# Performance work log

Measured on AMD Instinct MI355X. Metric: run time of the kernel, lower is better.

The kernel has to match this reference:

```python
import jax, jax.numpy as jnp
import numpy as np

D_MODEL = 768
N_HEADS = 12
CHUNK = 512
N_LM = 32
BATCH = 2
SEQ = 8192


def setup_inputs() -> dict:
    key = jax.random.key(0)
    ks = jax.random.split(key, 9)
    s = 1.0 / np.sqrt(D_MODEL)
    return {
        "x": jax.random.normal(ks[0], (BATCH, SEQ, D_MODEL), jnp.float32),
        "Wq": jax.random.normal(ks[1], (D_MODEL, D_MODEL), jnp.float32) * s,
        "bq": jax.random.normal(ks[2], (D_MODEL,), jnp.float32) * 0.01,
        "Wk": jax.random.normal(ks[3], (D_MODEL, D_MODEL), jnp.float32) * s,
        "bk": jax.random.normal(ks[4], (D_MODEL,), jnp.float32) * 0.01,
        "Wv": jax.random.normal(ks[5], (D_MODEL, D_MODEL), jnp.float32) * s,
        "bv": jax.random.normal(ks[6], (D_MODEL,), jnp.float32) * 0.01,
        "Wo": jax.random.normal(ks[7], (D_MODEL, D_MODEL), jnp.float32) * s,
        "bo": jax.random.normal(ks[8], (D_MODEL,), jnp.float32) * 0.01,
    }


def reference(x, Wq, bq, Wk, bk, Wv, bv, Wo, bo):
    B, S, D = x.shape
    H, hd = N_HEADS, D // N_HEADS
    scale = hd ** -0.5
    n_chunks = S // CHUNK  # SEQ chosen divisible by CHUNK -> no padding path

    # Global landmarks: mean-pool over N_LM evenly spaced segments
    seg = S // N_LM
    lm = x[:, : seg * N_LM, :].reshape(B, N_LM, seg, D).mean(axis=2)  # (B, L, D)

    # Q over local tokens only
    q = (x @ Wq.T + bq).reshape(B, n_chunks, CHUNK, H, hd)

    # K/V over [landmarks ++ local chunk]
    xc = x.reshape(B, n_chunks, CHUNK, D)
    lm_exp = jnp.broadcast_to(lm[:, None], (B, n_chunks, N_LM, D))
    kv = jnp.concatenate([lm_exp, xc], axis=2)  # (B, n_chunks, N_LM+CHUNK, D)
    k = (kv @ Wk.T + bk).reshape(B, n_chunks, N_LM + CHUNK, H, hd)
    v = (kv @ Wv.T + bv).reshape(B, n_chunks, N_LM + CHUNK, H, hd)

    attn = jnp.einsum("bnqhd,bnkhd->bnhqk", q, k) * scale
    attn = jax.nn.softmax(attn, axis=-1)  # dropout=0 (eval)
    out = jnp.einsum("bnhqk,bnkhd->bnqhd", attn, v).reshape(B, S, D)
    return out @ Wo.T + bo
```

## Files before the change

kernel.cpp:

```cpp
#include <hip/hip_runtime.h>
#include <cstdint>
#include <cstddef>

#define D_MODEL 768
#define N_HEADS 12
#define HEAD_DIM 64
#define CHUNK_SZ 512
#define N_LM 32
#define BATCH 2
#define SEQ 8192
#define N_CH 16
#define SEG 256
#define TOK (BATCH*SEQ)
#define MKV_PAD 16512
#define QSCALE 0.18033688011112042f
#define DEFER_THR 12.0f

typedef unsigned short u16;
typedef __attribute__((ext_vector_type(8))) __bf16 bf16x8;
typedef __attribute__((ext_vector_type(4))) float f32x4;

__device__ __forceinline__ u16 f2bf_rn(float f){
  union { __bf16 b; u16 u; } c; c.b = (__bf16)f; return c.u;
}

#define GLOAD_LDS16(gp, lp) \
  __builtin_amdgcn_global_load_lds((const __attribute__((address_space(1))) void*)(gp), \
                                   (__attribute__((address_space(3))) void*)(lp), 16, 0, 0)

__device__ __forceinline__ int xcd_remap(int bid, int nwg){
  int q = nwg >> 3, r = nwg & 7;
  int xcd = bid & 7, j = bid >> 3;
  return (xcd < r ? xcd*(q+1) : r*(q+1) + (xcd-r)*q) + j;
}

__global__ __launch_bounds__(256) void cvt4_kernel(
    const float* __restrict__ w0, const float* __restrict__ w1,
    const float* __restrict__ w2, const float* __restrict__ w3,
    u16* __restrict__ o0, u16* __restrict__ o1, u16* __restrict__ o2, u16* __restrict__ o3)
{
  const int n4 = D_MODEL*D_MODEL/4;
  int i = blockIdx.x*256 + threadIdx.x;
  int sel = i / n4, j = i - sel*n4;
  const float* s = sel==0 ? w0 : sel==1 ? w1 : sel==2 ? w2 : w3;
  u16* o = sel==0 ? o0 : sel==1 ? o1 : sel==2 ? o2 : o3;
  float4 v = reinterpret_cast<const float4*>(s)[j];
  ushort4 p; p.x=f2bf_rn(v.x); p.y=f2bf_rn(v.y); p.z=f2bf_rn(v.z); p.w=f2bf_rn(v.w);
  reinterpret_cast<ushort4*>(o)[j] = p;
}

__global__ void build_xcat_kernel(const float* __restrict__ x, u16* __restrict__ xcat){
  const int total4 = MKV_PAD * D_MODEL / 4;
  const int x4 = TOK * D_MODEL / 4;
  int stride = gridDim.x * blockDim.x;
  for (int i = blockIdx.x*blockDim.x + threadIdx.x; i < total4; i += stride){
    ushort4 o;
    if (i < x4){
      float4 v = reinterpret_cast<const float4*>(x)[i];
      o.x = f2bf_rn(v.x); o.y = f2bf_rn(v.y); o.z = f2bf_rn(v.z); o.w = f2bf_rn(v.w);
    } else { o.x = 0; o.y = 0; o.z = 0; o.w = 0; }
    reinterpret_cast<ushort4*>(xcat)[i] = o;
  }
}

__global__ __launch_bounds__(256) void lm_part_kernel(const float* __restrict__ x, float* __restrict__ lmp){
  int seg = blockIdx.x >> 3, sub = blockIdx.x & 7;
  int b = seg >> 5, l = seg & 31;
  const float* base = x + ((size_t)b*SEQ + (size_t)l*SEG + (size_t)sub*32) * D_MODEL;
  int d = threadIdx.x;
  float a0=0.f, a1=0.f, a2=0.f;
  for (int tt=0; tt<32; ++tt){
    const float* row = base + (size_t)tt*D_MODEL;
    a0 += row[d]; a1 += row[d+256]; a2 += row[d+512];
  }
  float* orow = lmp + (size_t)blockIdx.x * D_MODEL;
  orow[d] = a0; orow[d+256] = a1; orow[d+512] = a2;
}
__global__ __launch_bounds__(256) void lm_final_kernel(const float* __restrict__ lmp, u16* __restrict__ xcat){
  int seg = blockIdx.x;
  int d = threadIdx.x;
  float a0=0.f, a1=0.f, a2=0.f;
  #pragma unroll
  for (int i=0;i<8;i++){
    const float* p = lmp + ((size_t)seg*8 + i)*D_MODEL;
    a0 += p[d]; a1 += p[d+256]; a2 += p[d+512];
  }
  u16* orow = xcat + ((size_t)TOK + seg)*D_MODEL;
  const float inv = 1.f/(float)SEG;
  orow[d] = f2bf_rn(a0*inv); orow[d+256] = f2bf_rn(a1*inv); orow[d+512] = f2bf_rn(a2*inv);
}

#define GEMM_PROLOG                                                                \
  const int t = threadIdx.x;                                                       \
  const int lane = t & 63, wid = t >> 6;                                           \
  const int wr = wid >> 1, wc = wid & 1;                                           \
  const int lr = lane & 15, lg = lane >> 4;

#define GEMM_MAINLOOP(Aptr, Bptr)                                                  \
  __shared__ u16 As[2*128*64];                                                     \
  __shared__ u16 Bs[2*128*64];                                                     \
  const int srow = lane >> 3;                                                      \
  const int scolx = (((lane & 7) ^ (lane >> 3)) << 3);   \
  const u16* ga = (Aptr) + (row0 + srow)*(size_t)D_MODEL + scolx;                  \
  const u16* gb = (Bptr) + ((size_t)col0 + srow)*(size_t)D_MODEL + scolx;          \
  f32x4 acc[4][4];                                                                 \
  _Pragma("unroll") for (int m=0;m<4;m++)                                          \
    _Pragma("unroll") for (int n=0;n<4;n++) acc[m][n] = f32x4{0.f,0.f,0.f,0.f};    \
  {                                                                                \
    _Pragma("unroll") for (int i=0;i<4;i++){                                       \
      int chunk = wid*4 + i;                                                       \
      GLOAD_LDS16(ga + (size_t)chunk*8*D_MODEL, As + chunk*512);                   \
      GLOAD_LDS16(gb + (size_t)chunk*8*D_MODEL, Bs + chunk*512);                   \
    }                                                                              \
  }                                                                                \
  int cur = 0;                                                                     \
  const int rsw = (lr & 7) << 3;                                                   \
  for (int ts = 0; ts < D_MODEL/64; ++ts){                                         \
    __builtin_amdgcn_s_barrier();         \
    if (ts < D_MODEL/64 - 1){                                                      \
      int nb = (cur ^ 1) * 8192;                                                   \
      _Pragma("unroll") for (int i=0;i<4;i++){                                     \
        int chunk = wid*4 + i;                                                     \
        GLOAD_LDS16(ga + (size_t)chunk*8*D_MODEL + (ts+1)*64, As + nb + chunk*512);\
        GLOAD_LDS16(gb + (size_t)chunk*8*D_MODEL + (ts+1)*64, Bs + nb + chunk*512);\
      }                                                                            \
      asm volatile("s_waitcnt vmcnt(8)" ::: "memory");        \
    } else {                                                                       \
      asm volatile("s_waitcnt vmcnt(0)" ::: "memory");                             \
    }                                                                              \
    __builtin_amdgcn_s_barrier();              \
    __builtin_amdgcn_sched_barrier(0);                                             \
    int cb = cur * 8192;                                                           \
    _Pragma("unroll") for (int kk=0;kk<2;kk++){                                    \
      bf16x8 af[4], bv[4];                                                         \
      _Pragma("unroll") for (int m=0;m<4;m++)                                      \
        af[m] = *reinterpret_cast<const bf16x8*>(                                  \
            &As[cb + (wr*64 + m*16 + lr)*64 + ((kk*32 + lg*8) ^ rsw)]);            \
      _Pragma("unroll") for (int n=0;n<4;n++)                                      \
        bv[n] = *reinterpret_cast<const bf16x8*>(                                  \
            &Bs[cb + (wc*64 + n*16 + lr)*64 + ((kk*32 + lg*8) ^ rsw)]);            \
      _Pragma("unroll") for (int m=0;m<4;m++)                                      \
        _Pragma("unroll") for (int n=0;n<4;n++)                                    \
          acc[m][n] = __builtin_amdgcn_mfma_f32_16x16x32_bf16(af[m], bv[n], acc[m][n], 0, 0, 0); \
    }                                                                              \
    cur ^= 1;                                                                      \
  }

template<int OUT_F32, int BIAS_ROW, int ROWFAST, int NFAST>
__global__ __launch_bounds__(256) void gemm_bt_kernel(
    const u16* __restrict__ A, const u16* __restrict__ Bt,
    const float* __restrict__ bias, void* __restrict__ Cout, int ldc, float scale)
{
  int g = xcd_remap(blockIdx.x, gridDim.x);
  int rowt, colt;
  if (ROWFAST){ rowt = g % NFAST; colt = g / NFAST; }
  else        { colt = g % NFAST; rowt = g / NFAST; }
  const size_t row0 = (size_t)rowt * 128;
  const int col0 = colt * 128;
  GEMM_PROLOG
  GEMM_MAINLOOP(A, Bt)

  __syncthreads();
  if (OUT_F32){
    float* Fw = reinterpret_cast<float*>(wid < 2 ? As : Bs) + (wid & 1) * 4096;
    #pragma unroll
    for (int m=0;m<4;m++){
      #pragma unroll
      for (int n=0;n<4;n++){
        const int col = col0 + wc*64 + n*16 + lr;
        const float bcol = BIAS_ROW ? 0.f : bias[col];
        #pragma unroll
        for (int e=0;e<4;e++){
          size_t row = row0 + wr*64 + m*16 + lg*4 + e;
          float b = BIAS_ROW ? bias[row] : bcol;
          Fw[(m*16 + lg*4 + e)*64 + n*16 + lr] = (acc[m][n][e] + b) * scale;
        }
      }
    }
    __syncthreads();
    float* fo = reinterpret_cast<float*>(Cout);
    #pragma unroll
    for (int i=0;i<16;i++){
      int rr = i*4 + (lane >> 4), cc = (lane & 15) * 4;
      float4 v = *reinterpret_cast<const float4*>(&Fw[rr*64 + cc]);
      *reinterpret_cast<float4*>(&fo[(row0 + wr*64 + rr)*(size_t)ldc + col0 + wc*64 + cc]) = v;
    }
  } else {
    u16* Cw = (wid < 2 ? As : Bs) + (wid & 1) * 4608;
    #pragma unroll
    for (int m=0;m<4;m++){
      #pragma unroll
      for (int n=0;n<4;n++){
        const int col = col0 + wc*64 + n*16 + lr;
        const float bcol = BIAS_ROW ? 0.f : bias[col];
        #pragma unroll
        for (int e=0;e<4;e++){
          size_t row = row0 + wr*64 + m*16 + lg*4 + e;
          float b = BIAS_ROW ? bias[row] : bcol;
          Cw[(m*16 + lg*4 + e)*72 + n*16 + lr] = f2bf_rn((acc[m][n][e] + b) * scale);
        }
      }
    }
    __syncthreads();
    u16* uo = reinterpret_cast<u16*>(Cout);
    #pragma unroll
    for (int i=0;i<8;i++){
      int rr = i*8 + (lane >> 3), cc = (lane & 7) * 8;
      bf16x8 v = *reinterpret_cast<const bf16x8*>(&Cw[rr*72 + cc]);
      *reinterpret_cast<bf16x8*>(&uo[(row0 + wr*64 + rr)*(size_t)ldc + col0 + wc*64 + cc]) = v;
    }
  }
}

__global__ __launch_bounds__(256) void gemm_qk_kernel(
    const u16* __restrict__ A, const u16* __restrict__ Wqk,
    const float* __restrict__ bq, const float* __restrict__ bk,
    u16* __restrict__ Qb, u16* __restrict__ Kb)
{
  int g = xcd_remap(blockIdx.x, gridDim.x);
  int colt = g % 12, rowt = g / 12;
  const size_t row0 = (size_t)rowt * 128;
  const int col0 = colt * 128;
  GEMM_PROLOG
  GEMM_MAINLOOP(A, Wqk)

  const bool isk = col0 >= 768;
  const float scale = isk ? 1.f : QSCALE;
  u16* dst = isk ? Kb : Qb;
  const int ocol0 = isk ? col0 - 768 : col0;

  __syncthreads();
  u16* Cw = (wid < 2 ? As : Bs) + (wid & 1) * 4608;
  #pragma unroll
  for (int m=0;m<4;m++){
    #pragma unroll
    for (int n=0;n<4;n++){
      const int ocol = ocol0 + wc*64 + n*16 + lr;
      const float b = isk ? bk[ocol] : bq[ocol];
      #pragma unroll
      for (int e=0;e<4;e++)
        Cw[(m*16 + lg*4 + e)*72 + n*16 + lr] = f2bf_rn((acc[m][n][e] + b) * scale);
    }
  }
  __syncthreads();
  #pragma unroll
  for (int i=0;i<8;i++){
    int rr = i*8 + (lane >> 3), cc = (lane & 7) * 8;
    size_t grow = row0 + wr*64 + rr;
    if (isk || grow < TOK){
      bf16x8 v = *reinterpret_cast<const bf16x8*>(&Cw[rr*72 + cc]);
      *reinterpret_cast<bf16x8*>(&dst[grow*D_MODEL + ocol0 + wc*64 + cc]) = v;
    }
  }
}

template<int NK>
__device__ __forceinline__ void attn_compute(
    int lr, int lg,
    const u16 (* __restrict__ Ks)[72], const u16 (* __restrict__ Vs)[72],
    u16 (* __restrict__ Pw)[72],
    const bf16x8 (&qf)[2][2], float (&m_run)[2], float (&l_run)[2], f32x4 (&of)[2][4])
{
  constexpr int NCF = NK/16;
  constexpr int NKT = NK/32;

  f32x4 s2[2][NCF];
  #pragma unroll
  for (int c=0;c<NCF;c++){
    bf16x8 kf0 = *reinterpret_cast<const bf16x8*>(&Ks[c*16 + lr][lg*8]);
    bf16x8 kf1 = *reinterpret_cast<const bf16x8*>(&Ks[c*16 + lr][32 + lg*8]);
    #pragma unroll
    for (int r=0;r<2;r++){
      f32x4 s = f32x4{0.f,0.f,0.f,0.f};
      s = __builtin_amdgcn_mfma_f32_16x16x32_bf16(kf0, qf[r][0], s, 0,0,0);
      s = __builtin_amdgcn_mfma_f32_16x16x32_bf16(kf1, qf[r][1], s, 0,0,0);
      s2[r][c] = s;
    }
  }

  bf16x8 vf[NKT][4];
  #pragma unroll
  for (int kt=0;kt<NKT;kt++)
    #pragma unroll
    for (int c=0;c<4;c++)
      vf[kt][c] = *reinterpret_cast<const bf16x8*>(&Vs[c*16 + lr][kt*32 + lg*8]);

  #pragma unroll
  for (int r=0;r<2;r++){
    float tm = s2[r][0][0];
    #pragma unroll
    for (int c=0;c<NCF;c++)
      #pragma unroll
      for (int e=0;e<4;e++) tm = fmaxf(tm, s2[r][c][e]);
    tm = fmaxf(tm, __shfl_xor(tm, 16, 64));
    tm = fmaxf(tm, __shfl_xor(tm, 32, 64));
    if (!__all(tm - m_run[r] <= DEFER_THR)){
      float mnew = fmaxf(m_run[r], tm);
      float al = exp2f(m_run[r] - mnew);
      m_run[r] = mnew;
      l_run[r] *= al;
      #pragma unroll
      for (int c=0;c<4;c++)
        #pragma unroll
        for (int e=0;e<4;e++) of[r][c][e] *= al;
    }
    float ts = 0.f;
    #pragma unroll
    for (int c=0;c<NCF;c++)
      #pragma unroll
      for (int e=0;e<4;e++){
        float p = exp2f(s2[r][c][e] - m_run[r]);
        s2[r][c][e] = p;
        ts += p;
      }
    ts += __shfl_xor(ts, 16, 64);
    ts += __shfl_xor(ts, 32, 64);
    l_run[r] += ts;

    #pragma unroll
    for (int c=0;c<NCF;c++){
      ushort4 pk;
      pk.x = f2bf_rn(s2[r][c][0]); pk.y = f2bf_rn(s2[r][c][1]);
      pk.z = f2bf_rn(s2[r][c][2]); pk.w = f2bf_rn(s2[r][c][3]);
      *reinterpret_cast<ushort4*>(&Pw[lr][c*16 + lg*4]) = pk;
    }
    #pragma unroll
    for (int kt=0;kt<NKT;kt++){
      bf16x8 pf = *reinterpret_cast<const bf16x8*>(&Pw[lr][kt*32 + lg*8]);
      #pragma unroll
      for (int c=0;c<4;c++)
        of[r][c] = __builtin_amdgcn_mfma_f32_16x16x32_bf16(vf[kt][c], pf, of[r][c], 0,0,0);
    }
  }
}

__global__ __launch_bounds__(256) void attn_kernel(
    const u16* __restrict__ Qb, const u16* __restrict__ Kb,
    const u16* __restrict__ Vt, u16* __restrict__ AO)
{
  __shared__ u16 Ks[64][72];
  __shared__ u16 Vs[64][72];
  __shared__ u16 PwAll[4][16][72];

  const int t = threadIdx.x;
  const int lane = t & 63, w = t >> 6;
  const int lr = lane & 15, lg = lane >> 4;
  const int qt = blockIdx.x;
  const int h  = blockIdx.y;
  const int b  = blockIdx.z >> 4, ch = blockIdx.z & 15;
  const size_t tok0 = (size_t)b*SEQ + (size_t)ch*CHUNK_SZ + (size_t)qt*128;
  const size_t bch0 = (size_t)b*SEQ + (size_t)ch*CHUNK_SZ;
  u16 (* __restrict__ Pw)[72] = PwAll[w];

  bf16x8 qf[2][2];
  #pragma unroll
  for (int r=0;r<2;r++)
    #pragma unroll
    for (int kk=0;kk<2;kk++)
      qf[r][kk] = *reinterpret_cast<const bf16x8*>(
          &Qb[(tok0 + w*32 + r*16 + lr)*D_MODEL + (size_t)h*HEAD_DIM + kk*32 + lg*8]);

  float m_run[2] = {-INFINITY, -INFINITY};
  float l_run[2] = {0.f, 0.f};
  f32x4 of[2][4];
  #pragma unroll
  for (int r=0;r<2;r++)
    #pragma unroll
    for (int c=0;c<4;c++) of[r][c] = f32x4{0.f,0.f,0.f,0.f};

  {
    const size_t lmrow0 = (size_t)TOK + (size_t)b*N_LM;
    int key = t >> 3, dc = (t & 7) << 3;
    *reinterpret_cast<bf16x8*>(&Ks[key][dc]) = *reinterpret_cast<const bf16x8*>(
        &Kb[(lmrow0 + key)*D_MODEL + (size_t)h*HEAD_DIM + dc]);
    int d = t >> 2, kc = (t & 3) << 3;
    *reinterpret_cast<bf16x8*>(&Vs[d][kc]) = *reinterpret_cast<const bf16x8*>(
        &Vt[((size_t)h*HEAD_DIM + d)*MKV_PAD + lmrow0 + kc]);
    __syncthreads();
    attn_compute<32>(lr, lg, Ks, Vs, Pw, qf, m_run, l_run, of);
  }

  bf16x8 kreg[2], vreg[2];
  const int key0 = t >> 3, dc0 = (t & 7) << 3;
  const int d0 = t >> 3, kc0 = (t & 7) << 3;
  {
    size_t col0 = bch0;
    kreg[0] = *reinterpret_cast<const bf16x8*>(&Kb[(col0 + key0)*D_MODEL + (size_t)h*HEAD_DIM + dc0]);
    kreg[1] = *reinterpret_cast<const bf16x8*>(&Kb[(col0 + key0 + 32)*D_MODEL + (size_t)h*HEAD_DIM + dc0]);
    vreg[0] = *reinterpret_cast<const bf16x8*>(&Vt[((size_t)h*HEAD_DIM + d0)*MKV_PAD + col0 + kc0]);
    vreg[1] = *reinterpret_cast<const bf16x8*>(&Vt[((size_t)h*HEAD_DIM + d0 + 32)*MKV_PAD + col0 + kc0]);
  }
  for (int tl = 0; tl < 8; ++tl){
    __syncthreads();
    *reinterpret_cast<bf16x8*>(&Ks[key0][dc0])      = kreg[0];
    *reinterpret_cast<bf16x8*>(&Ks[key0 + 32][dc0]) = kreg[1];
    *reinterpret_cast<bf16x8*>(&Vs[d0][kc0])        = vreg[0];
    *reinterpret_cast<bf16x8*>(&Vs[d0 + 32][kc0])   = vreg[1];
    __syncthreads();
    if (tl < 7){
      size_t col0 = bch0 + (size_t)(tl+1)*64;
      kreg[0] = *reinterpret_cast<const bf16x8*>(&Kb[(col0 + key0)*D_MODEL + (size_t)h*HEAD_DIM + dc0]);
      kreg[1] = *reinterpret_cast<const bf16x8*>(&Kb[(col0 + key0 + 32)*D_MODEL + (size_t)h*HEAD_DIM + dc0]);
      vreg[0] = *reinterpret_cast<const bf16x8*>(&Vt[((size_t)h*HEAD_DIM + d0)*MKV_PAD + col0 + kc0]);
      vreg[1] = *reinterpret_cast<const bf16x8*>(&Vt[((size_t)h*HEAD_DIM + d0 + 32)*MKV_PAD + col0 + kc0]);
    }
    attn_compute<64>(lr, lg, Ks, Vs, Pw, qf, m_run, l_run, of);
  }

  #pragma unroll
  for (int r=0;r<2;r++){
    float inv = 1.f / l_run[r];
    size_t row = (tok0 + w*32 + r*16 + lr)*D_MODEL + (size_t)h*HEAD_DIM;
    #pragma unroll
    for (int c=0;c<4;c++){
      ushort4 pk;
      pk.x = f2bf_rn(of[r][c][0]*inv); pk.y = f2bf_rn(of[r][c][1]*inv);
      pk.z = f2bf_rn(of[r][c][2]*inv); pk.w = f2bf_rn(of[r][c][3]*inv);
      *reinterpret_cast<ushort4*>(&AO[row + c*16 + lg*4]) = pk;
    }
  }
}

extern "C" void kernel_launch(void* const* d_in, const int* in_sizes, int n_in,
                              void* d_out, int out_size, void* d_ws, size_t ws_size,
                              hipStream_t stream) {
  const float* x  = (const float*)d_in[0];
  const float* Wq = (const float*)d_in[1];
  const float* bq = (const float*)d_in[2];
  const float* Wk = (const float*)d_in[3];
  const float* bk = (const float*)d_in[4];
  const float* Wv = (const float*)d_in[5];
  const float* bv = (const float*)d_in[6];
  const float* Wo = (const float*)d_in[7];
  const float* bo = (const float*)d_in[8];
  float* out = (float*)d_out;

  const size_t XCAT_OFF = 0;
  const size_t Q_OFF    = 25362432;
  const size_t K_OFF    = 50528256;
  const size_t VT_OFF   = 75890688;
  const size_t AO_OFF   = 101253120;
  const size_t WQ_OFF   = 126418944;
  const size_t WK_OFF   = 127598592;
  const size_t WV_OFF   = 128778240;
  const size_t WO_OFF   = 129957888;
  const size_t TOTAL    = 131137536;
  if (ws_size < TOTAL) return;

  char* ws = (char*)d_ws;
  u16* xcat = (u16*)(ws + XCAT_OFF);
  u16* Qb   = (u16*)(ws + Q_OFF);
  u16* Kb   = (u16*)(ws + K_OFF);
  u16* Vt   = (u16*)(ws + VT_OFF);
  u16* AO   = (u16*)(ws + AO_OFF);
  float* lmp = (float*)(ws + AO_OFF);
  u16* wqkb = (u16*)(ws + WQ_OFF);
  u16* wkb  = (u16*)(ws + WK_OFF);
  u16* wvb  = (u16*)(ws + WV_OFF);
  u16* wob  = (u16*)(ws + WO_OFF);

  dim3 blk(256);
  cvt4_kernel<<<dim3(2304), blk, 0, stream>>>(Wq, Wk, Wv, Wo, wqkb, wkb, wvb, wob);
  build_xcat_kernel<<<dim3(4096), blk, 0, stream>>>(x, xcat);
  lm_part_kernel<<<dim3(512), blk, 0, stream>>>(x, lmp);
  lm_final_kernel<<<dim3(64), blk, 0, stream>>>(lmp, xcat);

  gemm_qk_kernel<<<dim3(1548), blk, 0, stream>>>(xcat, wqkb, bq, bk, Qb, Kb);
  gemm_bt_kernel<0,1,1,6><<<dim3(774), blk, 0, stream>>>(wvb, xcat, bv, (void*)Vt, MKV_PAD, 1.f);

  attn_kernel<<<dim3(4, 12, 32), blk, 0, stream>>>(Qb, Kb, Vt, AO);

  gemm_bt_kernel<1,0,0,6><<<dim3(768), blk, 0, stream>>>(AO, wob, bo, (void*)out, D_MODEL, 1.f);
}
```

Baseline: 228.5 us.

## Double-buffer K/V tiles via direct global-to-LDS loads with XOR swizzle

Replaces register-staged K/V tile loads with direct global-to-LDS loads (GLOAD_LDS16) into double-buffered, XOR-swizzled shared memory, synchronised with explicit vmcnt waits and raw barriers. The goal is to overlap the next tile's fetch with the current tile's compute, drop the register round-trip, and avoid LDS bank conflicts left by the old padded layout. It also raises wave priority around the MFMA sections. The trade-offs are more LDS use, which may lower occupancy, and reliance on hand-written waitcnt and barrier correctness.

```diff
diff --git a/kernel.cpp b/kernel.cpp
--- a/kernel.cpp
+++ b/kernel.cpp
@@ -257,18 +257,20 @@
 template<int NK>
 __device__ __forceinline__ void attn_compute(
     int lr, int lg,
-    const u16 (* __restrict__ Ks)[72], const u16 (* __restrict__ Vs)[72],
+    const u16* __restrict__ Ksb, const u16* __restrict__ Vsb,
     u16 (* __restrict__ Pw)[72],
     const bf16x8 (&qf)[2][2], float (&m_run)[2], float (&l_run)[2], f32x4 (&of)[2][4])
 {
   constexpr int NCF = NK/16;
   constexpr int NKT = NK/32;
+  const int rsw = (lr & 7) << 3;
 
   f32x4 s2[2][NCF];
+  __builtin_amdgcn_s_setprio(1);
   #pragma unroll
   for (int c=0;c<NCF;c++){
-    bf16x8 kf0 = *reinterpret_cast<const bf16x8*>(&Ks[c*16 + lr][lg*8]);
-    bf16x8 kf1 = *reinterpret_cast<const bf16x8*>(&Ks[c*16 + lr][32 + lg*8]);
+    bf16x8 kf0 = *reinterpret_cast<const bf16x8*>(&Ksb[(c*16 + lr)*64 + ((lg*8) ^ rsw)]);
+    bf16x8 kf1 = *reinterpret_cast<const bf16x8*>(&Ksb[(c*16 + lr)*64 + ((32 + lg*8) ^ rsw)]);
     #pragma unroll
     for (int r=0;r<2;r++){
       f32x4 s = f32x4{0.f,0.f,0.f,0.f};
@@ -277,13 +279,14 @@
       s2[r][c] = s;
     }
   }
+  __builtin_amdgcn_s_setprio(0);
 
   bf16x8 vf[NKT][4];
   #pragma unroll
   for (int kt=0;kt<NKT;kt++)
     #pragma unroll
     for (int c=0;c<4;c++)
-      vf[kt][c] = *reinterpret_cast<const bf16x8*>(&Vs[c*16 + lr][kt*32 + lg*8]);
+      vf[kt][c] = *reinterpret_cast<const bf16x8*>(&Vsb[(c*16 + lr)*64 + ((kt*32 + lg*8) ^ rsw)]);
 
   #pragma unroll
   for (int r=0;r<2;r++){
@@ -324,6 +327,7 @@
       pk.z = f2bf_rn(s2[r][c][2]); pk.w = f2bf_rn(s2[r][c][3]);
       *reinterpret_cast<ushort4*>(&Pw[lr][c*16 + lg*4]) = pk;
     }
+    __builtin_amdgcn_s_setprio(1);
     #pragma unroll
     for (int kt=0;kt<NKT;kt++){
       bf16x8 pf = *reinterpret_cast<const bf16x8*>(&Pw[lr][kt*32 + lg*8]);
@@ -331,6 +335,7 @@
       for (int c=0;c<4;c++)
         of[r][c] = __builtin_amdgcn_mfma_f32_16x16x32_bf16(vf[kt][c], pf, of[r][c], 0,0,0);
     }
+    __builtin_amdgcn_s_setprio(0);
   }
 }
 
@@ -338,8 +343,8 @@
     const u16* __restrict__ Qb, const u16* __restrict__ Kb,
     const u16* __restrict__ Vt, u16* __restrict__ AO)
 {
-  __shared__ u16 Ks[64][72];
-  __shared__ u16 Vs[64][72];
+  __shared__ u16 Ks[2*4096];
+  __shared__ u16 Vs[2*4096];
   __shared__ u16 PwAll[4][16][72];
 
   const int t = threadIdx.x;
@@ -371,41 +376,47 @@
   {
     const size_t lmrow0 = (size_t)TOK + (size_t)b*N_LM;
     int key = t >> 3, dc = (t & 7) << 3;
-    *reinterpret_cast<bf16x8*>(&Ks[key][dc]) = *reinterpret_cast<const bf16x8*>(
+    bf16x8 kv = *reinterpret_cast<const bf16x8*>(
         &Kb[(lmrow0 + key)*D_MODEL + (size_t)h*HEAD_DIM + dc]);
+    *reinterpret_cast<bf16x8*>(&Ks[key*64 + (dc ^ ((key & 7) << 3))]) = kv;
     int d = t >> 2, kc = (t & 3) << 3;
-    *reinterpret_cast<bf16x8*>(&Vs[d][kc]) = *reinterpret_cast<const bf16x8*>(
+    bf16x8 vv = *reinterpret_cast<const bf16x8*>(
         &Vt[((size_t)h*HEAD_DIM + d)*MKV_PAD + lmrow0 + kc]);
-    __syncthreads();
-    attn_compute<32>(lr, lg, Ks, Vs, Pw, qf, m_run, l_run, of);
-  }
-
-  bf16x8 kreg[2], vreg[2];
-  const int key0 = t >> 3, dc0 = (t & 7) << 3;
-  const int d0 = t >> 3, kc0 = (t & 7) << 3;
-  {
-    size_t col0 = bch0;
-    kreg[0] = *reinterpret_cast<const bf16x8*>(&Kb[(col0 + key0)*D_MODEL + (size_t)h*HEAD_DIM + dc0]);
-    kreg[1] = *reinterpret_cast<const bf16x8*>(&Kb[(col0 + key0 + 32)*D_MODEL + (size_t)h*HEAD_DIM + dc0]);
-    vreg[0] = *reinterpret_cast<const bf16x8*>(&Vt[((size_t)h*HEAD_DIM + d0)*MKV_PAD + col0 + kc0]);
-    vreg[1] = *reinterpret_cast<const bf16x8*>(&Vt[((size_t)h*HEAD_DIM + d0 + 32)*MKV_PAD + col0 + kc0]);
-  }
+    *reinterpret_cast<bf16x8*>(&Vs[d*64 + (kc ^ ((d & 7) << 3))]) = vv;
+  }
+  __syncthreads();
+
+  const int srow = lane >> 3;
+  const int scolx = ((lane & 7) ^ (lane >> 3)) << 3;
+  #define STAGE_KV(tile_, buf_) { \
+    size_t kb0 = bch0 + (size_t)(tile_)*64; \
+    _Pragma("unroll") for (int i_=0;i_<2;i_++){ \
+      int chunk_ = w*2 + i_; \
+      GLOAD_LDS16(Kb + (kb0 + (size_t)chunk_*8 + srow)*D_MODEL + (size_t)h*HEAD_DIM + scolx, \
+                  Ks + (buf_)*4096 + chunk_*512); \
+      GLOAD_LDS16(Vt + ((size_t)h*HEAD_DIM + chunk_*8 + srow)*MKV_PAD + kb0 + scolx, \
+                  Vs + (buf_)*4096 + chunk_*512); \
+    } }
+
+  STAGE_KV(0, 1)
+
+  attn_compute<32>(lr, lg, Ks, Vs, Pw, qf, m_run, l_run, of);
+
+  int cur = 1;
   for (int tl = 0; tl < 8; ++tl){
-    __syncthreads();
-    *reinterpret_cast<bf16x8*>(&Ks[key0][dc0])      = kreg[0];
-    *reinterpret_cast<bf16x8*>(&Ks[key0 + 32][dc0]) = kreg[1];
-    *reinterpret_cast<bf16x8*>(&Vs[d0][kc0])        = vreg[0];
-    *reinterpret_cast<bf16x8*>(&Vs[d0 + 32][kc0])   = vreg[1];
-    __syncthreads();
+    __builtin_amdgcn_s_barrier();
     if (tl < 7){
-      size_t col0 = bch0 + (size_t)(tl+1)*64;
-      kreg[0] = *reinterpret_cast<const bf16x8*>(&Kb[(col0 + key0)*D_MODEL + (size_t)h*HEAD_DIM + dc0]);
-      kreg[1] = *reinterpret_cast<const bf16x8*>(&Kb[(col0 + key0 + 32)*D_MODEL + (size_t)h*HEAD_DIM + dc0]);
-      vreg[0] = *reinterpret_cast<const bf16x8*>(&Vt[((size_t)h*HEAD_DIM + d0)*MKV_PAD + col0 + kc0]);
-      vreg[1] = *reinterpret_cast<const bf16x8*>(&Vt[((size_t)h*HEAD_DIM + d0 + 32)*MKV_PAD + col0 + kc0]);
-    }
-    attn_compute<64>(lr, lg, Ks, Vs, Pw, qf, m_run, l_run, of);
-  }
+      STAGE_KV(tl+1, cur^1)
+      asm volatile("s_waitcnt vmcnt(4)" ::: "memory");
+    } else {
+      asm volatile("s_waitcnt vmcnt(0)" ::: "memory");
+    }
+    __builtin_amdgcn_s_barrier();
+    __builtin_amdgcn_sched_barrier(0);
+    attn_compute<64>(lr, lg, Ks + cur*4096, Vs + cur*4096, Pw, qf, m_run, l_run, of);
+    cur ^= 1;
+  }
+  #undef STAGE_KV
 
   #pragma unroll
   for (int r=0;r<2;r++){
```

Result: slower. 237.5 us (+4.0%).
